# Performance work log

Hardware: AMD Instinct MI355X
Metric: run time of the kernel (lower is better)

The kernel has to match this reference:

```python
import jax, jax.numpy as jnp
import numpy as np

B, N, C, H = 2, 2048, 1024, 16
D = C // H  # head_dim = 64
EPS = 1e-6


def rmsnorm(x, w, eps=EPS):
    # RMSNorm over last dim (head_dim), matching torch RMSNorm (computed in fp32)
    x32 = x.astype(jnp.float32)
    y = x32 * jax.lax.rsqrt(jnp.mean(x32 * x32, axis=-1, keepdims=True) + eps)
    return y.astype(x.dtype) * w


def setup_inputs() -> dict:
    key = jax.random.key(0)
    ks = jax.random.split(key, 4)
    return {
        "x": jax.random.normal(ks[0], (B, N, C), dtype=jnp.float32),
        "w_qkv": jax.random.normal(ks[1], (C, 3 * C), dtype=jnp.float32) * 0.02,
        "b_qkv": jnp.zeros((3 * C,), dtype=jnp.float32),
        "q_w": jnp.ones((D,), dtype=jnp.float32),
        "k_w": jnp.ones((D,), dtype=jnp.float32),
        "w_proj": jax.random.normal(ks[2], (C, C), dtype=jnp.float32) * 0.02,
        "b_proj": jnp.zeros((C,), dtype=jnp.float32),
    }


def reference(x, w_qkv, b_qkv, q_w, k_w, w_proj, b_proj):
    b, n, c = x.shape
    h, d = H, c // H
    # QKV projection -> [3, B, H, N, D]
    qkv = (x @ w_qkv + b_qkv).reshape(b, n, 3, h, d).transpose(2, 0, 3, 1, 4)
    q, k, v = qkv[0], qkv[1], qkv[2]
    # per-head RMSNorm on q/k (qk_norm=True, use_rmsnorm=True)
    q = rmsnorm(q, q_w)
    k = rmsnorm(k, k_w)
    # scaled dot-product attention (scale = head_dim**-0.5, no dropout at eval)
    scale = d ** -0.5
    attn = jax.nn.softmax(jnp.einsum('bhqd,bhkd->bhqk', q, k) * scale, axis=-1)
    out = jnp.einsum('bhqk,bhkd->bhqd', attn, v)  # [B,H,N,D]
    out = out.transpose(0, 2, 1, 3).reshape(b, n, c)
    return out @ w_proj + b_proj
```

## Files before the change

### kernel.cpp

```cpp
#include <hip/hip_runtime.h>

typedef unsigned short u16;
typedef unsigned int u32;
typedef float f4 __attribute__((ext_vector_type(4)));
typedef __bf16 b8 __attribute__((ext_vector_type(8)));
typedef _Float16 h4 __attribute__((ext_vector_type(4)));
typedef __fp16 hp2 __attribute__((ext_vector_type(2)));

typedef const __attribute__((address_space(1))) u32 gu32;
typedef __attribute__((address_space(3))) u32 lu32;

#if __has_builtin(__builtin_amdgcn_exp2f)
#define EXP2(x) __builtin_amdgcn_exp2f(x)
#else
#define EXP2(x) exp2f(x)
#endif

__device__ __forceinline__ void gll16(const void* g, void* l) {
  __builtin_amdgcn_global_load_lds((gu32*)g, (lu32*)l, 16, 0, 0);
}

__device__ __forceinline__ u16 f2bf(float f) {
  unsigned u = __float_as_uint(f);
  u += 0x7fffu + ((u >> 16) & 1u);
  return (u16)(u >> 16);
}
__device__ __forceinline__ float bf2f(u16 h) {
  return __uint_as_float(((unsigned)h) << 16);
}

__global__ void k_convert_all(const float* __restrict__ x,
                              const float* __restrict__ w_qkv,
                              const float* __restrict__ w_proj,
                              u16* __restrict__ xb, u16* __restrict__ wqkT,
                              u16* __restrict__ wpjT) {
  __shared__ u16 t[64][65];
  int bid = blockIdx.x;
  if (bid < 2048) {
    int i = (bid * 256 + threadIdx.x) * 8;
    float4 a = *(const float4*)(x + i);
    float4 b = *(const float4*)(x + i + 4);
    union { u16 h[8]; uint4 v; } r;
    r.h[0] = f2bf(a.x); r.h[1] = f2bf(a.y); r.h[2] = f2bf(a.z); r.h[3] = f2bf(a.w);
    r.h[4] = f2bf(b.x); r.h[5] = f2bf(b.y); r.h[6] = f2bf(b.z); r.h[7] = f2bf(b.w);
    *(uint4*)(xb + i) = r.v;
    return;
  }
  const float* w; u16* wT; int Ncols, Krows, bx, by;
  if (bid < 2816) { int l = bid - 2048; w = w_qkv; wT = wqkT; Ncols = 3072; Krows = 1024; bx = l % 48; by = l / 48; }
  else            { int l = bid - 2816; w = w_proj; wT = wpjT; Ncols = 1024; Krows = 1024; bx = l & 15; by = l >> 4; }
  int n0 = bx * 64, k0 = by * 64;
#pragma unroll
  for (int it = 0; it < 16; ++it) {
    int e = it * 256 + threadIdx.x;
    int r = e >> 6, c = e & 63;
    t[r][c] = f2bf(w[(size_t)(k0 + r) * Ncols + n0 + c]);
  }
  __syncthreads();
#pragma unroll
  for (int it = 0; it < 16; ++it) {
    int e = it * 256 + threadIdx.x;
    int r = e >> 6, c = e & 63;
    wT[(size_t)(n0 + r) * Krows + k0 + c] = t[c][r];
  }
}

__global__ __launch_bounds__(256, 3) void k_gemm_qkv(
    const u16* __restrict__ A, const u16* __restrict__ Bt,
    const float* __restrict__ bias,
    u16* __restrict__ oq, u16* __restrict__ ok, u16* __restrict__ ov,
    const float* __restrict__ qw, const float* __restrict__ kw,
    int K) {
  __shared__ u16 lA[128 * 32];
  __shared__ u16 lB[128 * 32];
  const int tid = threadIdx.x;
  const int lane = tid & 63, lrow = lane & 15, lq = lane >> 4;
  const int wave = tid >> 6;
  const int bm = blockIdx.y * 128, bn = blockIdx.x * 128;
  const int wm = (wave >> 1) * 64, wn = (wave & 1) * 64;
  f4 acc[4][4] = {};
  for (int kb = 0; kb < K; kb += 32) {
#pragma unroll
    for (int s = 0; s < 2; ++s) {
      int cb = s * 256 + wave * 64;
      int ch = cb + lane;
      int row = ch >> 2, ko = (ch & 3) * 8;
      gll16(A + (size_t)(bm + row) * K + kb + ko, lA + cb * 8);
      gll16(Bt + (size_t)(bn + row) * K + kb + ko, lB + cb * 8);
    }
    __syncthreads();
    b8 af[4], bf[4];
#pragma unroll
    for (int i = 0; i < 4; ++i)
      af[i] = *(const b8*)(lA + (wm + i * 16 + lrow) * 32 + lq * 8);
#pragma unroll
    for (int j = 0; j < 4; ++j)
      bf[j] = *(const b8*)(lB + (wn + j * 16 + lrow) * 32 + lq * 8);
#pragma unroll
    for (int i = 0; i < 4; ++i)
#pragma unroll
      for (int j = 0; j < 4; ++j)
        acc[i][j] = __builtin_amdgcn_mfma_f32_16x16x32_bf16(af[i], bf[j], acc[i][j], 0, 0, 0);
    __syncthreads();
  }

  float bv[4];
#pragma unroll
  for (int j = 0; j < 4; ++j) bv[j] = bias[bn + wn + j * 16 + lrow];

  const float CS = 0.125f * 1.44269504088896340736f;
  const int n0w = bn + wn;
  const int sec = n0w >> 10;
  const int h = (n0w >> 6) & 15;
#pragma unroll
  for (int i = 0; i < 4; ++i) {
    float v[4][4];
#pragma unroll
    for (int j = 0; j < 4; ++j)
#pragma unroll
      for (int r = 0; r < 4; ++r) v[j][r] = acc[i][j][r] + bv[j];
    if (sec < 2) {
      u16* dst = sec == 0 ? oq : ok;
      const float* w = sec == 0 ? qw : kw;
      float ex = sec == 0 ? CS : 1.0f;
#pragma unroll
      for (int r = 0; r < 4; ++r) {
        float ss = v[0][r] * v[0][r] + v[1][r] * v[1][r] +
                   v[2][r] * v[2][r] + v[3][r] * v[3][r];
        ss += __shfl_xor(ss, 1, 64); ss += __shfl_xor(ss, 2, 64);
        ss += __shfl_xor(ss, 4, 64); ss += __shfl_xor(ss, 8, 64);
        float sc = rsqrtf(ss * (1.0f / 64.0f) + 1e-6f) * ex;
        int m = bm + wm + i * 16 + lq * 4 + r;
        int bb = m >> 11, ns = m & 2047;
        u16* rowp = dst + ((size_t)(bb * 16 + h) * 2048 + ns) * 64;
#pragma unroll
        for (int j = 0; j < 4; ++j) {
          int d = j * 16 + lrow;
          rowp[d] = f2bf(v[j][r] * sc * w[d]);
        }
      }
    } else {
      int m0 = bm + wm + i * 16 + lq * 4;
      int bb = m0 >> 11, ns = m0 & 2047;
#pragma unroll
      for (int j = 0; j < 4; ++j) {
        int d = j * 16 + lrow;
        union { _Float16 hh[4]; uint2 u; } pk;
#pragma unroll
        for (int r = 0; r < 4; ++r) pk.hh[r] = (_Float16)v[j][r];
        *(uint2*)(ov + ((size_t)(bb * 16 + h) * 64 + d) * 2048 + ns) = pk.u;
      }
    }
  }
}

__global__ __launch_bounds__(256, 4) void k_gemm2(
    const u16* __restrict__ A, const u16* __restrict__ Bt,
    const float* __restrict__ bias, float* __restrict__ outF,
    int K, int Ncols) {
  __shared__ u16 lA[64 * 32];
  __shared__ u16 lB[128 * 32];
  const int tid = threadIdx.x;
  const int lane = tid & 63, lrow = lane & 15, lq = lane >> 4;
  const int wave = tid >> 6;
  const int bm = blockIdx.y * 64, bn = blockIdx.x * 128;
  const int wm = (wave >> 1) * 32, wn = (wave & 1) * 64;
  f4 acc[2][4] = {};
  for (int kb = 0; kb < K; kb += 32) {
    {
      int cb = wave * 64;
      int ch = cb + lane;
      int row = ch >> 2, ko = (ch & 3) * 8;
      gll16(A + (size_t)(bm + row) * K + kb + ko, lA + cb * 8);
    }
#pragma unroll
    for (int s = 0; s < 2; ++s) {
      int cb = s * 256 + wave * 64;
      int ch = cb + lane;
      int row = ch >> 2, ko = (ch & 3) * 8;
      gll16(Bt + (size_t)(bn + row) * K + kb + ko, lB + cb * 8);
    }
    __syncthreads();
    b8 af[2], bf[4];
#pragma unroll
    for (int i = 0; i < 2; ++i)
      af[i] = *(const b8*)(lA + (wm + i * 16 + lrow) * 32 + lq * 8);
#pragma unroll
    for (int j = 0; j < 4; ++j)
      bf[j] = *(const b8*)(lB + (wn + j * 16 + lrow) * 32 + lq * 8);
#pragma unroll
    for (int i = 0; i < 2; ++i)
#pragma unroll
      for (int j = 0; j < 4; ++j)
        acc[i][j] = __builtin_amdgcn_mfma_f32_16x16x32_bf16(af[i], bf[j], acc[i][j], 0, 0, 0);
    __syncthreads();
  }
#pragma unroll
  for (int i = 0; i < 2; ++i)
#pragma unroll
    for (int j = 0; j < 4; ++j) {
      int n = bn + wn + j * 16 + lrow;
      float bv = bias[n];
#pragma unroll
      for (int r = 0; r < 4; ++r) {
        int m = bm + wm + i * 16 + lq * 4 + r;
        outF[(size_t)m * Ncols + n] = acc[i][j][r] + bv;
      }
    }
}

__global__ __launch_bounds__(512, 4) void k_attn(
    const u16* __restrict__ qb, const u16* __restrict__ kb,
    const u16* __restrict__ vt, u16* __restrict__ ao) {
  __shared__ u16 lK[128 * 72];
  __shared__ u16 lV[64 * 140];
  const int bh = blockIdx.y;
  const int q0 = blockIdx.x * 128;
  const int tid = threadIdx.x, wave = tid >> 6, lane = tid & 63;
  const int lrow = lane & 15, lq = lane >> 4;
  const int wq = wave * 16;

  b8 qf[2];
#pragma unroll
  for (int ks = 0; ks < 2; ++ks)
    qf[ks] = *(const b8*)(qb + ((size_t)bh * 2048 + q0 + wq + lrow) * 64 + ks * 32 + lq * 8);

  f4 o[4] = {};
  f4 lacc = {};
  h4 ones;
  ones[0] = (_Float16)1.0f; ones[1] = (_Float16)1.0f;
  ones[2] = (_Float16)1.0f; ones[3] = (_Float16)1.0f;

  const int ch0 = tid, ch1 = 512 + tid;
  const u16* kp0 = kb + (size_t)bh * 2048 * 64 + (size_t)(ch0 >> 3) * 64 + (ch0 & 7) * 8;
  const u16* kp1 = kb + (size_t)bh * 2048 * 64 + (size_t)(ch1 >> 3) * 64 + (ch1 & 7) * 8;
  const u16* vp0 = vt + (size_t)bh * 64 * 2048 + (size_t)(ch0 >> 4) * 2048 + (ch0 & 15) * 8;
  const u16* vp1 = vt + (size_t)bh * 64 * 2048 + (size_t)(ch1 >> 4) * 2048 + (ch1 & 15) * 8;
  u16* lKw0 = lK + (ch0 >> 3) * 72 + (ch0 & 7) * 8;
  u16* lKw1 = lK + (ch1 >> 3) * 72 + (ch1 & 7) * 8;
  u16* lVw0 = lV + (ch0 >> 4) * 140 + (ch0 & 15) * 8;
  u16* lVw1 = lV + (ch1 >> 4) * 140 + (ch1 & 15) * 8;

  uint4 pK0, pK1, pV0, pV1;
  pK0 = *(const uint4*)kp0; pK1 = *(const uint4*)kp1;
  pV0 = *(const uint4*)vp0; pV1 = *(const uint4*)vp1;

  for (int it = 0; it < 16; ++it) {
    *(uint4*)lKw0 = pK0;
    *(uint4*)lKw1 = pK1;
    *(uint2*)lVw0 = make_uint2(pV0.x, pV0.y);
    *(uint2*)(lVw0 + 4) = make_uint2(pV0.z, pV0.w);
    *(uint2*)lVw1 = make_uint2(pV1.x, pV1.y);
    *(uint2*)(lVw1 + 4) = make_uint2(pV1.z, pV1.w);
    __syncthreads();

    if (it < 15) {
      kp0 += 128 * 64; kp1 += 128 * 64; vp0 += 128; vp1 += 128;
      pK0 = *(const uint4*)kp0; pK1 = *(const uint4*)kp1;
      pV0 = *(const uint4*)vp0; pV1 = *(const uint4*)vp1;
    }

    f4 st[8] = {};
#pragma unroll
    for (int ks = 0; ks < 2; ++ks)
#pragma unroll
      for (int kt = 0; kt < 8; ++kt) {
        b8 kf = *(const b8*)(lK + (kt * 16 + lrow) * 72 + ks * 32 + lq * 8);
        st[kt] = __builtin_amdgcn_mfma_f32_16x16x32_bf16(kf, qf[ks], st[kt], 0, 0, 0);
      }

    h4 pf[8];
#pragma unroll
    for (int kt = 0; kt < 8; ++kt) {
      union { hp2 p2[2]; h4 v; } cv;
      cv.p2[0] = __builtin_amdgcn_cvt_pkrtz(EXP2(st[kt][0]), EXP2(st[kt][1]));
      cv.p2[1] = __builtin_amdgcn_cvt_pkrtz(EXP2(st[kt][2]), EXP2(st[kt][3]));
      pf[kt] = cv.v;
    }

#pragma unroll
    for (int kt = 0; kt < 8; ++kt) {
      lacc = __builtin_amdgcn_mfma_f32_16x16x16f16(ones, pf[kt], lacc, 0, 0, 0);
#pragma unroll
      for (int dt = 0; dt < 4; ++dt) {
        h4 va = *(const h4*)(lV + (dt * 16 + lrow) * 140 + kt * 16 + lq * 4);
        o[dt] = __builtin_amdgcn_mfma_f32_16x16x16f16(va, pf[kt], o[dt], 0, 0, 0);
      }
    }
    __syncthreads();
  }

  float inv = 1.0f / lacc[0];

  const int bb = bh >> 4, h = bh & 15;
  int q = q0 + wq + lrow;
#pragma unroll
  for (int dt = 0; dt < 4; ++dt) {
    union { u16 h2[4]; uint2 v; } r;
#pragma unroll
    for (int rr = 0; rr < 4; ++rr) r.h2[rr] = f2bf(o[dt][rr] * inv);
    *(uint2*)(ao + ((size_t)bb * 2048 + q) * 1024 + h * 64 + dt * 16 + lq * 4) = r.v;
  }
}

extern "C" void kernel_launch(void* const* d_in, const int* in_sizes, int n_in,
                              void* d_out, int out_size, void* d_ws, size_t ws_size,
                              hipStream_t stream) {
  const float* x      = (const float*)d_in[0];
  const float* w_qkv  = (const float*)d_in[1];
  const float* b_qkv  = (const float*)d_in[2];
  const float* q_w    = (const float*)d_in[3];
  const float* k_w    = (const float*)d_in[4];
  const float* w_proj = (const float*)d_in[5];
  const float* b_proj = (const float*)d_in[6];
  float* out = (float*)d_out;

  u16* xb   = (u16*)d_ws;
  u16* wqkT = xb + 4194304;
  u16* wpjT = wqkT + 3145728;
  u16* qb   = wpjT + 1048576;
  u16* kb   = qb + 4194304;
  u16* vtb  = kb + 4194304;
  u16* ao   = xb;

  k_convert_all<<<3072, 256, 0, stream>>>(x, w_qkv, w_proj, xb, wqkT, wpjT);
  k_gemm_qkv<<<dim3(24, 32), 256, 0, stream>>>(xb, wqkT, b_qkv, qb, kb, vtb, q_w, k_w, 1024);
  k_attn<<<dim3(16, 32), 512, 0, stream>>>(qb, kb, vtb, ao);
  k_gemm2<<<dim3(8, 64), 256, 0, stream>>>(ao, wpjT, b_proj, out, 1024, 1024);
}
```

Measured before the change: 193.4 us.

## Prefetch GEMM tiles into registers instead of direct global-to-LDS loads

```diff
diff --git a/kernel.cpp b/kernel.cpp
--- a/kernel.cpp
+++ b/kernel.cpp
@@ -7,18 +7,11 @@
 typedef _Float16 h4 __attribute__((ext_vector_type(4)));
 typedef __fp16 hp2 __attribute__((ext_vector_type(2)));
 
-typedef const __attribute__((address_space(1))) u32 gu32;
-typedef __attribute__((address_space(3))) u32 lu32;
-
 #if __has_builtin(__builtin_amdgcn_exp2f)
 #define EXP2(x) __builtin_amdgcn_exp2f(x)
 #else
 #define EXP2(x) exp2f(x)
 #endif
-
-__device__ __forceinline__ void gll16(const void* g, void* l) {
-  __builtin_amdgcn_global_load_lds((gu32*)g, (lu32*)l, 16, 0, 0);
-}
 
 __device__ __forceinline__ u16 f2bf(float f) {
   unsigned u = __float_as_uint(f);
@@ -78,17 +71,29 @@
   const int wave = tid >> 6;
   const int bm = blockIdx.y * 128, bn = blockIdx.x * 128;
   const int wm = (wave >> 1) * 64, wn = (wave & 1) * 64;
+
+  const int ch0 = tid, ch1 = 256 + tid;
+  const u16* ap0 = A + (size_t)(bm + (ch0 >> 2)) * K + (ch0 & 3) * 8;
+  const u16* ap1 = A + (size_t)(bm + (ch1 >> 2)) * K + (ch1 & 3) * 8;
+  const u16* bp0 = Bt + (size_t)(bn + (ch0 >> 2)) * K + (ch0 & 3) * 8;
+  const u16* bp1 = Bt + (size_t)(bn + (ch1 >> 2)) * K + (ch1 & 3) * 8;
+  u16* lAw0 = lA + ch0 * 8; u16* lAw1 = lA + ch1 * 8;
+  u16* lBw0 = lB + ch0 * 8; u16* lBw1 = lB + ch1 * 8;
+
+  uint4 pA0 = *(const uint4*)ap0, pA1 = *(const uint4*)ap1;
+  uint4 pB0 = *(const uint4*)bp0, pB1 = *(const uint4*)bp1;
+
   f4 acc[4][4] = {};
-  for (int kb = 0; kb < K; kb += 32) {
-#pragma unroll
-    for (int s = 0; s < 2; ++s) {
-      int cb = s * 256 + wave * 64;
-      int ch = cb + lane;
-      int row = ch >> 2, ko = (ch & 3) * 8;
-      gll16(A + (size_t)(bm + row) * K + kb + ko, lA + cb * 8);
-      gll16(Bt + (size_t)(bn + row) * K + kb + ko, lB + cb * 8);
-    }
-    __syncthreads();
+  const int iters = K >> 5;
+  for (int it = 0; it < iters; ++it) {
+    *(uint4*)lAw0 = pA0; *(uint4*)lAw1 = pA1;
+    *(uint4*)lBw0 = pB0; *(uint4*)lBw1 = pB1;
+    __syncthreads();
+    if (it + 1 < iters) {
+      ap0 += 32; ap1 += 32; bp0 += 32; bp1 += 32;
+      pA0 = *(const uint4*)ap0; pA1 = *(const uint4*)ap1;
+      pB0 = *(const uint4*)bp0; pB1 = *(const uint4*)bp1;
+    }
     b8 af[4], bf[4];
 #pragma unroll
     for (int i = 0; i < 4; ++i)
@@ -165,22 +170,29 @@
   const int wave = tid >> 6;
   const int bm = blockIdx.y * 64, bn = blockIdx.x * 128;
   const int wm = (wave >> 1) * 32, wn = (wave & 1) * 64;
+
+  const int cha = tid;
+  const int ch0 = tid, ch1 = 256 + tid;
+  const u16* ap = A + (size_t)(bm + (cha >> 2)) * K + (cha & 3) * 8;
+  const u16* bp0 = Bt + (size_t)(bn + (ch0 >> 2)) * K + (ch0 & 3) * 8;
+  const u16* bp1 = Bt + (size_t)(bn + (ch1 >> 2)) * K + (ch1 & 3) * 8;
+  u16* lAw = lA + cha * 8;
+  u16* lBw0 = lB + ch0 * 8; u16* lBw1 = lB + ch1 * 8;
+
+  uint4 pA = *(const uint4*)ap;
+  uint4 pB0 = *(const uint4*)bp0, pB1 = *(const uint4*)bp1;
+
   f4 acc[2][4] = {};
-  for (int kb = 0; kb < K; kb += 32) {
-    {
-      int cb = wave * 64;
-      int ch = cb + lane;
-      int row = ch >> 2, ko = (ch & 3) * 8;
-      gll16(A + (size_t)(bm + row) * K + kb + ko, lA + cb * 8);
-    }
-#pragma unroll
-    for (int s = 0; s < 2; ++s) {
-      int cb = s * 256 + wave * 64;
-      int ch = cb + lane;
-      int row = ch >> 2, ko = (ch & 3) * 8;
-      gll16(Bt + (size_t)(bn + row) * K + kb + ko, lB + cb * 8);
-    }
-    __syncthreads();
+  const int iters = K >> 5;
+  for (int it = 0; it < iters; ++it) {
+    *(uint4*)lAw = pA;
+    *(uint4*)lBw0 = pB0; *(uint4*)lBw1 = pB1;
+    __syncthreads();
+    if (it + 1 < iters) {
+      ap += 32; bp0 += 32; bp1 += 32;
+      pA = *(const uint4*)ap;
+      pB0 = *(const uint4*)bp0; pB1 = *(const uint4*)bp1;
+    }
     b8 af[2], bf[4];
 #pragma unroll
     for (int i = 0; i < 2; ++i)
```

After: 193.3 us. Within noise of the previous version (-0.1%).
